# Performance work log

Measured on AMD Instinct MI355X. Metric: run time of the kernel, lower is better.

## Reference

```python
import jax, jax.numpy as jnp
import numpy as np

H = 768
NH = 12
HD = H // NH
EPS = 1e-12


def setup_inputs() -> dict:
    key = jax.random.key(0)
    ks = jax.random.split(key, 12)
    B, S = 4, 1024
    scale = 0.02
    return {
        "hidden_states": jax.random.normal(ks[0], (B, S, H), jnp.float32),
        "rel_pos": jax.random.normal(ks[1], (B, NH, S, S), jnp.float32),
        "rel_2d_pos": jax.random.normal(ks[2], (B, NH, S, S), jnp.float32),
        "Wq": jax.random.normal(ks[3], (H, H), jnp.float32) * scale,
        "bq": jnp.zeros((H,), jnp.float32),
        "Wk": jax.random.normal(ks[4], (H, H), jnp.float32) * scale,
        "bk": jnp.zeros((H,), jnp.float32),
        "Wv": jax.random.normal(ks[5], (H, H), jnp.float32) * scale,
        "bv": jnp.zeros((H,), jnp.float32),
        "Wo": jax.random.normal(ks[6], (H, H), jnp.float32) * scale,
        "bo": jnp.zeros((H,), jnp.float32),
        "ln_g": jnp.ones((H,), jnp.float32),
        "ln_b": jnp.zeros((H,), jnp.float32),
    }


def reference(hidden_states, rel_pos, rel_2d_pos, Wq, bq, Wk, bk, Wv, bv, Wo, bo, ln_g, ln_b):
    B, S, _ = hidden_states.shape
    # qkv projections -> [B, S, NH, HD]
    q = (hidden_states @ Wq + bq).reshape(B, S, NH, HD)
    k = (hidden_states @ Wk + bk).reshape(B, S, NH, HD)
    v = (hidden_states @ Wv + bv).reshape(B, S, NH, HD)
    q = q / jnp.sqrt(jnp.asarray(HD, q.dtype))
    # attention scores [B, NH, S, S] + relative/spatial biases
    scores = jnp.einsum("bshd,bthd->bhst", q, k) + rel_pos + rel_2d_pos
    probs = jax.nn.softmax(scores.astype(jnp.float32), axis=-1).astype(v.dtype)
    # context [B, S, NH, HD] -> [B, S, H]
    ctx = jnp.einsum("bhst,bthd->bshd", probs, v).reshape(B, S, H)
    # self-output: dense + residual + LayerNorm
    y = ctx @ Wo + bo + hidden_states
    mu = jnp.mean(y, axis=-1, keepdims=True)
    var = jnp.mean((y - mu) ** 2, axis=-1, keepdims=True)
    out = (y - mu) * jax.lax.rsqrt(var + EPS) * ln_g + ln_b
    return out
```

## Files before the change

kernel.cpp:

```cpp
#include <hip/hip_runtime.h>

#define H 768
#define NH 12
#define HD 64
#define BB 4
#define SS 1024
#define MM (BB*SS)

typedef __bf16 bf16;
typedef __bf16 bf16x8 __attribute__((ext_vector_type(8)));
typedef __bf16 bf16x4 __attribute__((ext_vector_type(4)));
typedef float  f32x4  __attribute__((ext_vector_type(4)));

static __device__ __forceinline__ f32x4 mfma16(bf16x8 a, bf16x8 b, f32x4 c){
  return __builtin_amdgcn_mfma_f32_16x16x32_bf16(a, b, c, 0, 0, 0);
}

__global__ __launch_bounds__(256) void prep_hs(const float* __restrict__ hs, bf16* __restrict__ hsb){
  size_t i = (size_t)blockIdx.x*256 + threadIdx.x;
  f32x4 v = *(const f32x4*)(hs + i*4);
  bf16x4 o;
  #pragma unroll
  for(int j=0;j<4;j++) o[j] = (bf16)v[j];
  *(bf16x4*)(hsb + i*4) = o;
}

__global__ __launch_bounds__(256) void prep_wt(const float* __restrict__ Wq, const float* __restrict__ Wk,
                                               const float* __restrict__ Wv, const float* __restrict__ Wo,
                                               bf16* __restrict__ oq, bf16* __restrict__ ok,
                                               bf16* __restrict__ ov, bf16* __restrict__ oo){
  int z = blockIdx.z;
  const float* W = (z==0)?Wq:(z==1)?Wk:(z==2)?Wv:Wo;
  bf16* O = (z==0)?oq:(z==1)?ok:(z==2)?ov:oo;
  __shared__ float tile[64][65];
  int t = threadIdx.x;
  int k0 = blockIdx.y*64, n0 = blockIdx.x*64;
  #pragma unroll
  for(int i=0;i<4;i++){
    int idx = i*256+t; int r = idx>>4; int c4 = (idx&15)*4;
    f32x4 v = *(const f32x4*)(W + (size_t)(k0+r)*H + n0 + c4);
    tile[r][c4+0]=v[0]; tile[r][c4+1]=v[1]; tile[r][c4+2]=v[2]; tile[r][c4+3]=v[3];
  }
  __syncthreads();
  #pragma unroll
  for(int i=0;i<4;i++){
    int idx = i*256+t; int r = idx>>4; int c4 = (idx&15)*4;
    bf16x4 o;
    #pragma unroll
    for(int j=0;j<4;j++) o[j] = (bf16)tile[c4+j][r];
    *(bf16x4*)(O + (size_t)(n0+r)*H + k0 + c4) = o;
  }
}

__global__ __launch_bounds__(256) void qkv_gemm(const bf16* __restrict__ hsb,
    const bf16* __restrict__ wqT, const bf16* __restrict__ wkT, const bf16* __restrict__ wvT,
    const float* __restrict__ bq, const float* __restrict__ bk, const float* __restrict__ bv,
    bf16* __restrict__ qb, bf16* __restrict__ kb, bf16* __restrict__ vb){
  int t = threadIdx.x;
  int m0 = blockIdx.x*64;
  int by = blockIdx.y;
  int mat = by/12, nb = by%12, n0 = nb*64;
  const bf16* wT   = (mat==0)?wqT:(mat==1)?wkT:wvT;
  const float* bias= (mat==0)?bq :(mat==1)?bk :bv;
  bf16* outp       = (mat==0)?qb :(mat==1)?kb :vb;
  float scale      = (mat==0)?0.125f:1.0f;

  __shared__ __align__(16) bf16 As[64*40];
  __shared__ __align__(16) bf16 Bs[64*40];
  int lane=t&63, w=t>>6, g=lane>>4, c=lane&15;
  f32x4 acc[4] = {};
  int ar = t>>2, asg = (t&3)*8;
  for(int kt=0; kt<24; kt++){
    __syncthreads();
    *(bf16x8*)&As[ar*40+asg] = *(const bf16x8*)(hsb + (size_t)(m0+ar)*H + kt*32 + asg);
    *(bf16x8*)&Bs[ar*40+asg] = *(const bf16x8*)(wT  + (size_t)(n0+ar)*H + kt*32 + asg);
    __syncthreads();
    bf16x8 a = *(const bf16x8*)&As[(16*w+c)*40 + g*8];
    #pragma unroll
    for(int ct=0;ct<4;ct++){
      bf16x8 b = *(const bf16x8*)&Bs[(16*ct+c)*40 + g*8];
      acc[ct] = mfma16(a, b, acc[ct]);
    }
  }
  #pragma unroll
  for(int ct=0;ct<4;ct++){
    #pragma unroll
    for(int r=0;r<4;r++){
      int row = m0 + 16*w + 4*g + r;
      int col = 16*ct + c;
      float val = (acc[ct][r] + bias[n0+col]) * scale;
      int b_ = row>>10, s = row&1023;
      outp[(((size_t)(b_*NH + nb))*SS + s)*HD + col] = (bf16)val;
    }
  }
}

__global__ __launch_bounds__(256,3) void attn_kernel(const bf16* __restrict__ qbuf,
    const bf16* __restrict__ kbuf, const bf16* __restrict__ vbuf,
    const float* __restrict__ relp, const float* __restrict__ rel2,
    bf16* __restrict__ ctxb){
  int t = threadIdx.x;
  int qt = blockIdx.x, h = blockIdx.y, b_ = blockIdx.z;
  int q0 = qt*64;
  const bf16* qh = qbuf + ((size_t)(b_*NH+h))*SS*HD;
  const bf16* kh = kbuf + ((size_t)(b_*NH+h))*SS*HD;
  const bf16* vh = vbuf + ((size_t)(b_*NH+h))*SS*HD;
  const float* r1 = relp + ((size_t)(b_*NH+h))*SS*SS;
  const float* r2 = rel2 + ((size_t)(b_*NH+h))*SS*SS;

  __shared__ __align__(16) bf16 Ks[64*64];
  __shared__ __align__(16) bf16 Vs[64*64];
  __shared__ __align__(16) bf16 Ps[4][1024];
  __shared__ __align__(16) float relS[64][68];

  int lane=t&63, w=t>>6, g=lane>>4, c=lane&15;

  bf16x8 aq[2];
  {
    int qrow = q0 + 16*w + c;
    aq[0] = *(const bf16x8*)(qh + (size_t)qrow*HD + g*8);
    aq[1] = *(const bf16x8*)(qh + (size_t)qrow*HD + 32 + g*8);
  }

  int srow = t>>4, scol = (t&15)*4;
  const float* p1 = r1 + (size_t)(q0 + srow)*SS + scol;
  const float* p2 = r2 + (size_t)(q0 + srow)*SS + scol;

  int ks_s = t>>3, ks_seg = t&7;
  int ks_lds = ks_s*64 + ((ks_seg ^ (ks_s&7))<<3);

  f32x4 rr1[4], rr2[4];
  bf16x8 kreg[2], vreg[2];

  kreg[0] = *(const bf16x8*)(kh + (size_t)ks_s*HD + ks_seg*8);
  kreg[1] = *(const bf16x8*)(kh + (size_t)(32+ks_s)*HD + ks_seg*8);
  vreg[0] = *(const bf16x8*)(vh + (size_t)lane*HD + w*8);
  vreg[1] = *(const bf16x8*)(vh + (size_t)lane*HD + (4+w)*8);
  #pragma unroll
  for(int i=0;i<4;i++){
    rr1[i] = *(const f32x4*)(p1 + (size_t)i*16*SS);
    rr2[i] = *(const f32x4*)(p2 + (size_t)i*16*SS);
  }

  f32x4 cacc[4] = {};
  float m_r[4], l_r[4];
  #pragma unroll
  for(int r=0;r<4;r++){ m_r[r] = -1e30f; l_r[r] = 0.f; }

  for(int kt=0; kt<16; kt++){
    int knext = (kt<15 ? kt+1 : 15)*64;

    #pragma unroll
    for(int i=0;i<4;i++){
      f32x4 s = rr1[i] + rr2[i];
      *(f32x4*)&relS[i*16 + srow][scol] = s;
    }
    *(bf16x8*)&Ks[ks_lds]         = kreg[0];
    *(bf16x8*)&Ks[32*64 + ks_lds] = kreg[1];
    #pragma unroll
    for(int j=0;j<8;j++){
      Vs[(w*8+j)*64     + (lane ^ (j<<3))] = vreg[0][j];
      Vs[((4+w)*8+j)*64 + (lane ^ (j<<3))] = vreg[1][j];
    }

    kreg[0] = *(const bf16x8*)(kh + (size_t)(knext+ks_s)*HD + ks_seg*8);
    kreg[1] = *(const bf16x8*)(kh + (size_t)(knext+32+ks_s)*HD + ks_seg*8);
    vreg[0] = *(const bf16x8*)(vh + (size_t)(knext+lane)*HD + w*8);
    vreg[1] = *(const bf16x8*)(vh + (size_t)(knext+lane)*HD + (4+w)*8);
    #pragma unroll
    for(int i=0;i<4;i++){
      rr1[i] = *(const f32x4*)(p1 + (size_t)i*16*SS + knext);
      rr2[i] = *(const f32x4*)(p2 + (size_t)i*16*SS + knext);
    }
    __builtin_amdgcn_sched_barrier(0);

    asm volatile("s_waitcnt lgkmcnt(0)" ::: "memory");
    __builtin_amdgcn_s_barrier();

    f32x4 sc[4] = {};
    #pragma unroll
    for(int ks=0; ks<2; ks++){
      #pragma unroll
      for(int ct=0;ct<4;ct++){
        int scol_ = 16*ct + c;
        int seg = g + 4*ks;
        bf16x8 bk_ = *(const bf16x8*)&Ks[scol_*64 + ((seg ^ (scol_&7))<<3)];
        sc[ct] = mfma16(aq[ks], bk_, sc[ct]);
      }
    }
    #pragma unroll
    for(int ct=0;ct<4;ct++)
      #pragma unroll
      for(int r=0;r<4;r++)
        sc[ct][r] += relS[16*w + 4*g + r][16*ct + c];

    float mv[4];
    #pragma unroll
    for(int r=0;r<4;r++){
      float m2 = fmaxf(fmaxf(sc[0][r],sc[1][r]), fmaxf(sc[2][r],sc[3][r]));
      #pragma unroll
      for(int mk=1; mk<16; mk<<=1) m2 = fmaxf(m2, __shfl_xor(m2, mk));
      mv[r] = m2;
    }
    float grow = fmaxf(fmaxf(mv[0]-m_r[0], mv[1]-m_r[1]),
                       fmaxf(mv[2]-m_r[2], mv[3]-m_r[3]));
    if(!__all(grow <= 8.0f)){
      #pragma unroll
      for(int r=0;r<4;r++){
        float mn = fmaxf(m_r[r], mv[r]);
        float corr = __expf(m_r[r] - mn);
        m_r[r] = mn;
        l_r[r] *= corr;
        #pragma unroll
        for(int ct=0;ct<4;ct++) cacc[ct][r] *= corr;
      }
    }
    #pragma unroll
    for(int r=0;r<4;r++){
      float ls = 0.f;
      #pragma unroll
      for(int ct=0;ct<4;ct++){ float pp = __expf(sc[ct][r]-m_r[r]); sc[ct][r]=pp; ls += pp; }
      l_r[r] += ls;
    }
    #pragma unroll
    for(int ct=0;ct<4;ct++)
      #pragma unroll
      for(int r=0;r<4;r++){
        int row = 4*g + r, col = 16*ct + c;
        Ps[w][row*64 + (col ^ ((row&7)<<3))] = (bf16)sc[ct][r];
      }
    #pragma unroll
    for(int ks=0;ks<2;ks++){
      int seg = g + 4*ks;
      bf16x8 pa = *(const bf16x8*)&Ps[w][c*64 + ((seg ^ (c&7))<<3)];
      #pragma unroll
      for(int ct=0;ct<4;ct++){
        int d = 16*ct + c;
        bf16x8 bv_ = *(const bf16x8*)&Vs[d*64 + ((seg ^ (d&7))<<3)];
        cacc[ct] = mfma16(pa, bv_, cacc[ct]);
      }
    }
    __builtin_amdgcn_s_barrier();
  }

  #pragma unroll
  for(int r=0;r<4;r++){
    float ls = l_r[r];
    #pragma unroll
    for(int mk=1; mk<16; mk<<=1) ls += __shfl_xor(ls, mk);
    l_r[r] = 1.f/ls;
  }
  #pragma unroll
  for(int ct=0;ct<4;ct++)
    #pragma unroll
    for(int r=0;r<4;r++){
      int row = q0 + 16*w + 4*g + r;
      int col = 16*ct + c;
      float o = cacc[ct][r] * l_r[r];
      ctxb[((size_t)(b_*SS + row))*H + h*HD + col] = (bf16)o;
    }
}

__global__ __launch_bounds__(256) void out_gemm(const bf16* __restrict__ ctxb, const bf16* __restrict__ woT,
    const float* __restrict__ bo, const float* __restrict__ hs, float* __restrict__ y){
  int t = threadIdx.x;
  int m0 = blockIdx.x*64, n0 = blockIdx.y*64;
  __shared__ __align__(16) bf16 As[64*40];
  __shared__ __align__(16) bf16 Bs[64*40];
  int lane=t&63, w=t>>6, g=lane>>4, c=lane&15;
  f32x4 acc[4] = {};
  int ar = t>>2, asg = (t&3)*8;
  for(int kt=0; kt<24; kt++){
    __syncthreads();
    *(bf16x8*)&As[ar*40+asg] = *(const bf16x8*)(ctxb + (size_t)(m0+ar)*H + kt*32 + asg);
    *(bf16x8*)&Bs[ar*40+asg] = *(const bf16x8*)(woT  + (size_t)(n0+ar)*H + kt*32 + asg);
    __syncthreads();
    bf16x8 a = *(const bf16x8*)&As[(16*w+c)*40 + g*8];
    #pragma unroll
    for(int ct=0;ct<4;ct++){
      bf16x8 b = *(const bf16x8*)&Bs[(16*ct+c)*40 + g*8];
      acc[ct] = mfma16(a, b, acc[ct]);
    }
  }
  #pragma unroll
  for(int ct=0;ct<4;ct++)
    #pragma unroll
    for(int r=0;r<4;r++){
      int row = m0 + 16*w + 4*g + r;
      int col = n0 + 16*ct + c;
      y[(size_t)row*H + col] = acc[ct][r] + bo[col] + hs[(size_t)row*H + col];
    }
}

__global__ __launch_bounds__(256) void ln_kernel(const float* __restrict__ y,
    const float* __restrict__ gw, const float* __restrict__ bw, float* __restrict__ out){
  int row = blockIdx.x; int t = threadIdx.x;
  const float* yr = y + (size_t)row*H;
  float v0 = yr[t], v1 = yr[t+256], v2 = yr[t+512];
  float s = v0+v1+v2;
  #pragma unroll
  for(int mk=1; mk<64; mk<<=1) s += __shfl_xor(s, mk);
  __shared__ float red[8];
  int w = t>>6, lane = t&63;
  if(lane==0) red[w] = s;
  __syncthreads();
  float mu = (red[0]+red[1]+red[2]+red[3]) * (1.f/768.f);
  float d0=v0-mu, d1=v1-mu, d2=v2-mu;
  float s2 = d0*d0+d1*d1+d2*d2;
  #pragma unroll
  for(int mk=1; mk<64; mk<<=1) s2 += __shfl_xor(s2, mk);
  __syncthreads();
  if(lane==0) red[w] = s2;
  __syncthreads();
  float var = (red[0]+red[1]+red[2]+red[3]) * (1.f/768.f);
  float inv = rsqrtf(var + 1e-12f);
  out[(size_t)row*H + t]     = d0*inv*gw[t]     + bw[t];
  out[(size_t)row*H + t+256] = d1*inv*gw[t+256] + bw[t+256];
  out[(size_t)row*H + t+512] = d2*inv*gw[t+512] + bw[t+512];
}

extern "C" void kernel_launch(void* const* d_in, const int* in_sizes, int n_in,
                              void* d_out, int out_size, void* d_ws, size_t ws_size,
                              hipStream_t stream){
  const float* hs   = (const float*)d_in[0];
  const float* relp = (const float*)d_in[1];
  const float* rel2 = (const float*)d_in[2];
  const float* Wq   = (const float*)d_in[3];
  const float* bq   = (const float*)d_in[4];
  const float* Wk   = (const float*)d_in[5];
  const float* bk   = (const float*)d_in[6];
  const float* Wv   = (const float*)d_in[7];
  const float* bv   = (const float*)d_in[8];
  const float* Wo   = (const float*)d_in[9];
  const float* bo   = (const float*)d_in[10];
  const float* lng  = (const float*)d_in[11];
  const float* lnb  = (const float*)d_in[12];
  float* out = (float*)d_out;

  char* p = (char*)d_ws;
  bf16* hsb = (bf16*)p; p += (size_t)MM*H*2;
  bf16* wqT = (bf16*)p; p += (size_t)H*H*2;
  bf16* wkT = (bf16*)p; p += (size_t)H*H*2;
  bf16* wvT = (bf16*)p; p += (size_t)H*H*2;
  bf16* woT = (bf16*)p; p += (size_t)H*H*2;
  bf16* qbuf = (bf16*)p; p += (size_t)MM*H*2;
  bf16* kbuf = (bf16*)p; p += (size_t)MM*H*2;
  bf16* vbuf = (bf16*)p; p += (size_t)MM*H*2;
  bf16* ctxb = (bf16*)p; p += (size_t)MM*H*2;
  float* y   = (float*)p; p += (size_t)MM*H*4;

  prep_hs<<<dim3((MM*H/4)/256), 256, 0, stream>>>(hs, hsb);
  prep_wt<<<dim3(12,12,4), 256, 0, stream>>>(Wq, Wk, Wv, Wo, wqT, wkT, wvT, woT);
  qkv_gemm<<<dim3(64,36), 256, 0, stream>>>(hsb, wqT, wkT, wvT, bq, bk, bv, qbuf, kbuf, vbuf);
  attn_kernel<<<dim3(16,12,4), 256, 0, stream>>>(qbuf, kbuf, vbuf, relp, rel2, ctxb);
  out_gemm<<<dim3(64,12), 256, 0, stream>>>(ctxb, woT, bo, hs, y);
  ln_kernel<<<dim3(MM), 256, 0, stream>>>(y, lng, lnb, out);
}
```

Baseline: 181.9 us.

## Fuse output projection with LayerNorm and stream relative-bias loads nontemporally

Merges the output GEMM and the LayerNorm kernel into one kernel. Each block owns 16 full rows across all 768 columns and computes mean and variance in registers and LDS, which removes the fp32 intermediate y and one launch. Separately, the attention kernel now loads rel_pos and rel_2d_pos with nontemporal hints so that single-use data does not pollute the cache. In exchange, each block reloads the whole Wo tile set per k-step, which costs 61KB of LDS and heavy redundant global traffic. Only 256 blocks run with 12 accumulators per thread. Variance is computed as E[x^2]-mu^2, which is less numerically stable.

```diff
diff --git a/kernel.cpp b/kernel.cpp
--- a/kernel.cpp
+++ b/kernel.cpp
@@ -138,8 +138,8 @@
   vreg[1] = *(const bf16x8*)(vh + (size_t)lane*HD + (4+w)*8);
   #pragma unroll
   for(int i=0;i<4;i++){
-    rr1[i] = *(const f32x4*)(p1 + (size_t)i*16*SS);
-    rr2[i] = *(const f32x4*)(p2 + (size_t)i*16*SS);
+    rr1[i] = __builtin_nontemporal_load((const f32x4*)(p1 + (size_t)i*16*SS));
+    rr2[i] = __builtin_nontemporal_load((const f32x4*)(p2 + (size_t)i*16*SS));
   }
 
   f32x4 cacc[4] = {};
@@ -169,8 +169,8 @@
     vreg[1] = *(const bf16x8*)(vh + (size_t)(knext+lane)*HD + (4+w)*8);
     #pragma unroll
     for(int i=0;i<4;i++){
-      rr1[i] = *(const f32x4*)(p1 + (size_t)i*16*SS + knext);
-      rr2[i] = *(const f32x4*)(p2 + (size_t)i*16*SS + knext);
+      rr1[i] = __builtin_nontemporal_load((const f32x4*)(p1 + (size_t)i*16*SS + knext));
+      rr2[i] = __builtin_nontemporal_load((const f32x4*)(p2 + (size_t)i*16*SS + knext));
     }
     __builtin_amdgcn_sched_barrier(0);
 
@@ -261,62 +261,81 @@
     }
 }
 
-__global__ __launch_bounds__(256) void out_gemm(const bf16* __restrict__ ctxb, const bf16* __restrict__ woT,
-    const float* __restrict__ bo, const float* __restrict__ hs, float* __restrict__ y){
+__global__ __launch_bounds__(256) void out_ln(const bf16* __restrict__ ctxb, const bf16* __restrict__ woT,
+    const float* __restrict__ bo, const float* __restrict__ hs,
+    const float* __restrict__ gw, const float* __restrict__ bw,
+    float* __restrict__ out){
   int t = threadIdx.x;
-  int m0 = blockIdx.x*64, n0 = blockIdx.y*64;
-  __shared__ __align__(16) bf16 As[64*40];
-  __shared__ __align__(16) bf16 Bs[64*40];
+  int m0 = blockIdx.x*16;
+  __shared__ __align__(16) bf16 As[16*40];
+  __shared__ __align__(16) bf16 Bs[768*40];
+  __shared__ float redS[4][16];
+  __shared__ float redQ[4][16];
   int lane=t&63, w=t>>6, g=lane>>4, c=lane&15;
-  f32x4 acc[4] = {};
-  int ar = t>>2, asg = (t&3)*8;
+  f32x4 acc[12] = {};
+
   for(int kt=0; kt<24; kt++){
     __syncthreads();
-    *(bf16x8*)&As[ar*40+asg] = *(const bf16x8*)(ctxb + (size_t)(m0+ar)*H + kt*32 + asg);
-    *(bf16x8*)&Bs[ar*40+asg] = *(const bf16x8*)(woT  + (size_t)(n0+ar)*H + kt*32 + asg);
+    if(t < 64){
+      int row = t>>2, seg = (t&3)*8;
+      *(bf16x8*)&As[row*40+seg] = *(const bf16x8*)(ctxb + (size_t)(m0+row)*H + kt*32 + seg);
+    }
+    #pragma unroll
+    for(int i=0;i<12;i++){
+      int idx = i*256+t; int row = idx>>2; int seg = (idx&3)*8;
+      *(bf16x8*)&Bs[row*40+seg] = *(const bf16x8*)(woT + (size_t)row*H + kt*32 + seg);
+    }
     __syncthreads();
-    bf16x8 a = *(const bf16x8*)&As[(16*w+c)*40 + g*8];
-    #pragma unroll
-    for(int ct=0;ct<4;ct++){
-      bf16x8 b = *(const bf16x8*)&Bs[(16*ct+c)*40 + g*8];
+    bf16x8 a = *(const bf16x8*)&As[c*40 + g*8];
+    #pragma unroll
+    for(int ct=0;ct<12;ct++){
+      bf16x8 b = *(const bf16x8*)&Bs[(w*192 + 16*ct + c)*40 + g*8];
       acc[ct] = mfma16(a, b, acc[ct]);
     }
   }
-  #pragma unroll
-  for(int ct=0;ct<4;ct++)
-    #pragma unroll
-    for(int r=0;r<4;r++){
-      int row = m0 + 16*w + 4*g + r;
-      int col = n0 + 16*ct + c;
-      y[(size_t)row*H + col] = acc[ct][r] + bo[col] + hs[(size_t)row*H + col];
-    }
-}
-
-__global__ __launch_bounds__(256) void ln_kernel(const float* __restrict__ y,
-    const float* __restrict__ gw, const float* __restrict__ bw, float* __restrict__ out){
-  int row = blockIdx.x; int t = threadIdx.x;
-  const float* yr = y + (size_t)row*H;
-  float v0 = yr[t], v1 = yr[t+256], v2 = yr[t+512];
-  float s = v0+v1+v2;
-  #pragma unroll
-  for(int mk=1; mk<64; mk<<=1) s += __shfl_xor(s, mk);
-  __shared__ float red[8];
-  int w = t>>6, lane = t&63;
-  if(lane==0) red[w] = s;
+
+  #pragma unroll
+  for(int ct=0;ct<12;ct++){
+    int col = w*192 + 16*ct + c;
+    float bov = bo[col];
+    #pragma unroll
+    for(int r=0;r<4;r++){
+      int row = m0 + 4*g + r;
+      acc[ct][r] += bov + hs[(size_t)row*H + col];
+    }
+  }
+
+  float s1[4], s2[4];
+  #pragma unroll
+  for(int r=0;r<4;r++){
+    float a1 = 0.f, a2 = 0.f;
+    #pragma unroll
+    for(int ct=0;ct<12;ct++){ float v = acc[ct][r]; a1 += v; a2 += v*v; }
+    #pragma unroll
+    for(int mk=1; mk<16; mk<<=1){ a1 += __shfl_xor(a1, mk); a2 += __shfl_xor(a2, mk); }
+    s1[r] = a1; s2[r] = a2;
+  }
+  if(c == 0){
+    #pragma unroll
+    for(int r=0;r<4;r++){ redS[w][4*g+r] = s1[r]; redQ[w][4*g+r] = s2[r]; }
+  }
   __syncthreads();
-  float mu = (red[0]+red[1]+red[2]+red[3]) * (1.f/768.f);
-  float d0=v0-mu, d1=v1-mu, d2=v2-mu;
-  float s2 = d0*d0+d1*d1+d2*d2;
-  #pragma unroll
-  for(int mk=1; mk<64; mk<<=1) s2 += __shfl_xor(s2, mk);
-  __syncthreads();
-  if(lane==0) red[w] = s2;
-  __syncthreads();
-  float var = (red[0]+red[1]+red[2]+red[3]) * (1.f/768.f);
-  float inv = rsqrtf(var + 1e-12f);
-  out[(size_t)row*H + t]     = d0*inv*gw[t]     + bw[t];
-  out[(size_t)row*H + t+256] = d1*inv*gw[t+256] + bw[t+256];
-  out[(size_t)row*H + t+512] = d2*inv*gw[t+512] + bw[t+512];
+
+  #pragma unroll
+  for(int r=0;r<4;r++){
+    int rl = 4*g + r;
+    float tot1 = redS[0][rl] + redS[1][rl] + redS[2][rl] + redS[3][rl];
+    float tot2 = redQ[0][rl] + redQ[1][rl] + redQ[2][rl] + redQ[3][rl];
+    float mu  = tot1 * (1.f/768.f);
+    float var = tot2 * (1.f/768.f) - mu*mu;
+    float inv = rsqrtf(var + 1e-12f);
+    int row = m0 + rl;
+    #pragma unroll
+    for(int ct=0;ct<12;ct++){
+      int col = w*192 + 16*ct + c;
+      out[(size_t)row*H + col] = (acc[ct][r] - mu)*inv*gw[col] + bw[col];
+    }
+  }
 }
 
 extern "C" void kernel_launch(void* const* d_in, const int* in_sizes, int n_in,
@@ -338,21 +357,19 @@
   float* out = (float*)d_out;
 
   char* p = (char*)d_ws;
-  bf16* hsb = (bf16*)p; p += (size_t)MM*H*2;
-  bf16* wqT = (bf16*)p; p += (size_t)H*H*2;
-  bf16* wkT = (bf16*)p; p += (size_t)H*H*2;
-  bf16* wvT = (bf16*)p; p += (size_t)H*H*2;
-  bf16* woT = (bf16*)p; p += (size_t)H*H*2;
+  bf16* hsb  = (bf16*)p; p += (size_t)MM*H*2;
+  bf16* wqT  = (bf16*)p; p += (size_t)H*H*2;
+  bf16* wkT  = (bf16*)p; p += (size_t)H*H*2;
+  bf16* wvT  = (bf16*)p; p += (size_t)H*H*2;
+  bf16* woT  = (bf16*)p; p += (size_t)H*H*2;
   bf16* qbuf = (bf16*)p; p += (size_t)MM*H*2;
   bf16* kbuf = (bf16*)p; p += (size_t)MM*H*2;
   bf16* vbuf = (bf16*)p; p += (size_t)MM*H*2;
   bf16* ctxb = (bf16*)p; p += (size_t)MM*H*2;
-  float* y   = (float*)p; p += (size_t)MM*H*4;
 
   prep_hs<<<dim3((MM*H/4)/256), 256, 0, stream>>>(hs, hsb);
   prep_wt<<<dim3(12,12,4), 256, 0, stream>>>(Wq, Wk, Wv, Wo, wqT, wkT, wvT, woT);
   qkv_gemm<<<dim3(64,36), 256, 0, stream>>>(hsb, wqT, wkT, wvT, bq, bk, bv, qbuf, kbuf, vbuf);
   attn_kernel<<<dim3(16,12,4), 256, 0, stream>>>(qbuf, kbuf, vbuf, relp, rel2, ctxb);
-  out_gemm<<<dim3(64,12), 256, 0, stream>>>(ctxb, woT, bo, hs, y);
-  ln_kernel<<<dim3(MM), 256, 0, stream>>>(y, lng, lnb, out);
-}
+  out_ln<<<dim3(MM/16), 256, 0, stream>>>(ctxb, woT, bo, hs, lng, lnb, out);
+}
```

New measurement: 185.8 us. +2.2%, slower.
